# Performance work log

Hardware: AMD Instinct MI355X
Metric: run time of the kernel (lower is better)

Reference implementation:

```python
import math
import jax
import jax.numpy as jnp
import numpy as np
from jax import lax

D_MODEL = 256
N = 64
L = 2048
BATCH = 8
DT = 0.1


def setup_inputs() -> dict:
    key = jax.random.key(0)
    k1, k2, k3, k4 = jax.random.split(key, 4)
    n2 = N // 2
    # Faithful parameter init from _init_parameters
    A_real = jnp.log(jnp.ones((D_MODEL, n2), jnp.float32) * 0.5)
    A_imag = jnp.broadcast_to(jnp.arange(n2, dtype=jnp.float32) * math.pi, (D_MODEL, n2))
    C_real = jax.random.normal(k1, (D_MODEL, n2), jnp.float32)
    C_imag = jax.random.normal(k2, (D_MODEL, n2), jnp.float32)
    D = jnp.zeros((D_MODEL,), jnp.float32)
    u = jax.random.normal(k3, (BATCH, L, D_MODEL), jnp.float32)
    return {"u": u, "A_real": A_real, "A_imag": A_imag,
            "C_real": C_real, "C_imag": C_imag, "D": D}


def reference(u, A_real, A_imag, C_real, C_imag, D):
    batch, Lseq, d_model = u.shape
    # A = -exp(A_real) + i*A_imag ; discretize: A_disc = exp(A * dt)
    A = (-jnp.exp(A_real) + 1j * A_imag).astype(jnp.complex64)
    A_disc = jnp.exp(A * DT)  # (d, n/2) complex
    C = (C_real + 1j * C_imag).astype(jnp.complex64)  # (d, n/2)
    # torch.fft.rfftfreq(2L, 1/L) = arange(L+1) / 2
    freqs = jnp.arange(Lseq + 1, dtype=jnp.float32) * 0.5
    omega = jnp.exp((-2j * math.pi) * freqs.astype(jnp.complex64) / Lseq)  # (L+1,)
    # Cauchy-like sum over modes: (d, n/2, L+1) -> (d, L+1)
    k_f = (C[:, :, None] / (1.0 - omega[None, None, :] * A_disc[:, :, None])).sum(axis=1)
    # irfft to length 2L, keep first L taps -> depthwise conv kernel (d, L)
    k = jnp.fft.irfft(k_f, n=2 * Lseq, axis=-1)[:, :Lseq].astype(u.dtype)
    pad_left = (Lseq - 1) // 2
    pad_right =Seq = Lseq // 2
    uT = jnp.transpose(u, (0, 2, 1))  # (B, d, L)
    # torch conv1d == cross-correlation == lax conv (no kernel flip)
    y = lax.conv_general_dilated(
        uT, k[:, None, :],  # (d, 1, L) depthwise kernel
        window_strides=(1,), padding=[(pad_left, pad_right)],
        feature_group_count=d_model,
        dimension_numbers=("NCH", "OIH", "NCH"))
    y = y + D[None, :, None]
    return jnp.transpose(y, (0, 2, 1))  # (B, L, d)
```

## Files before the change

kernel.cpp:

```cpp
#include <hip/hip_runtime.h>
#include <hip/hip_bf16.h>
#include <math.h>

#define LSEQ   2048
#define DMODEL 256
#define NHALF  32
#define TMAX   1024
#define TM2    384
#define KPAD   16
#define KROWS  (LSEQ + 2*KPAD)
#define TT     16

typedef __attribute__((ext_vector_type(8))) short short8;
typedef __attribute__((ext_vector_type(4))) float f32x4;
typedef __attribute__((ext_vector_type(4))) unsigned int u32x4;

#define U3STR   2120
#define U3SH    (8*U3STR)
#define U3BYTES (U3SH*2)
#define KSLOT_STR 8848
#define OFF_K    U3BYTES
#define SMEM_F3  (OFF_K + 8*KSLOT_STR)
#define KBF_SH   4400
#define YTR_SMEM (64*260*4)
#define UIMG_SHORTS ((size_t)DMODEL*U3SH)
#define KBF_OFF_SH  UIMG_SHORTS
#define YT_OFF_B    ((UIMG_SHORTS + (size_t)DMODEL*KBF_SH)*2)
#define WS_NEED3    (YT_OFF_B + (size_t)8*LSEQ*DMODEL*4)

#define PB_CT0 0
#define PB_CT1 4928
#define PB_HRE 9856
#define PB_HIE 11392
#define PB_HIO 12160
#define PB_P   12928
#define PB_Q   17280
#define PB_C   23808
#define PB_BYTES 33792

__global__ __launch_bounds__(512, 2) void s4d_prep(
    const float* __restrict__ u,
    const float* __restrict__ A_real, const float* __restrict__ A_imag,
    const float* __restrict__ C_real, const float* __restrict__ C_imag,
    unsigned short* __restrict__ uimg, unsigned short* __restrict__ kbf)
{
    __shared__ __align__(16) unsigned char pbuf[PB_BYTES];
    const int tid = threadIdx.x;

    if (blockIdx.y < 8) {
        unsigned short (*tr)[66] = (unsigned short (*)[66])pbuf;
        const int m0 = blockIdx.x * 64;
        const int b  = blockIdx.y;

        const int mmBase = tid >> 6;
        const int d4     = (tid & 63) * 4;
        #pragma unroll
        for (int it = 0; it < 8; ++it) {
            int mm = it*8 + mmBase;
            const float* src = u + ((size_t)b*LSEQ + m0 + mm)*DMODEL + d4;
            f32x4 v = *(const f32x4*)src;
            #pragma unroll
            for (int j = 0; j < 4; ++j) {
                __hip_bfloat16 hb = __float2bfloat16(v[j]);
                tr[d4+j][mm] = *(unsigned short*)&hb;
            }
        }
        __syncthreads();
        #pragma unroll
        for (int P = 0; P < 4; ++P) {
            int d = P*64 + (tid >> 3);
            int c = tid & 7;
            const unsigned short* s = &tr[d][c*8];
            u32x4 w = { *(const unsigned*)(s),   *(const unsigned*)(s+2),
                        *(const unsigned*)(s+4), *(const unsigned*)(s+6) };
            *(u32x4*)(uimg + (size_t)d*U3SH + (size_t)b*U3STR + 32 + m0 + c*8) = w;
        }
        if (blockIdx.x == 0 && tid < 256) {
            int d = tid;
            #pragma unroll
            for (int c = 0; c < 4; ++c)
                *(u32x4*)(uimg + (size_t)d*U3SH + (size_t)b*U3STR + c*8) = (u32x4){0,0,0,0};
        } else if (blockIdx.x == 31 && tid < 256) {
            int d = tid;
            #pragma unroll
            for (int c = 0; c < 5; ++c)
                *(u32x4*)(uimg + (size_t)d*U3SH + (size_t)b*U3STR + 2080 + c*8) = (u32x4){0,0,0,0};
        }
    } else {
        const int d = (blockIdx.y - 8)*32 + blockIdx.x;
        float* ctL0 = (float*)(pbuf + PB_CT0);
        float* ctL1 = (float*)(pbuf + PB_CT1);
        float* hRe  = (float*)(pbuf + PB_HRE);
        float* hImE = (float*)(pbuf + PB_HIE);
        float* hImO = (float*)(pbuf + PB_HIO);
        float* Pp   = (float*)(pbuf + PB_P);
        float* Qp   = (float*)(pbuf + PB_Q);
        float* Cp   = (float*)(pbuf + PB_C);

        for (int i = tid; i < 1220; i += 512) {
            int x0 = (i - 196) & 2047;
            int x1 = (i - 195) & 2047;
            float a0 = (float)(M_PI/(2.0*(double)LSEQ)) * (float)(2*x0 + 1);
            float a1 = (float)(M_PI/(2.0*(double)LSEQ)) * (float)(2*x1 + 1);
            float s0, c0, s1, c1;
            sincosf(a0, &s0, &c0);
            sincosf(a1, &s1, &c1);
            ctL0[i] = c0 / s0;
            ctL1[i] = c1 / s1;
        }
        if (tid < 32) {
            const int n = tid;
            float ar = A_real[d*NHALF + n], ai = A_imag[d*NHALF + n];
            float cr = C_real[d*NHALF + n], ci = C_imag[d*NHALF + n];
            float amp = expf(-0.1f * expf(ar));
            float sn, cs; sincosf(0.1f * ai, &sn, &cs);
            float Adr = amp*cs, Adi = amp*sn;
            float pr = 1.f, pi = 0.f;
            Pp[n*2] = pr; Pp[n*2 + 1] = pi;
            #pragma unroll
            for (int i = 1; i < 16; ++i) {
                float nr = pr*Adr - pi*Adi;
                float ni = pr*Adi + pi*Adr;
                pr = nr; pi = ni;
                Pp[i*68 + n*2] = pr; Pp[i*68 + n*2 + 1] = pi;
            }
            float a16r = pr*Adr - pi*Adi;
            float a16i = pr*Adi + pi*Adr;
            float qr = 1.f, qi = 0.f;
            Qp[n*2] = qr; Qp[n*2 + 1] = qi;
            #pragma unroll
            for (int j = 1; j < 24; ++j) {
                float nr = qr*a16r - qi*a16i;
                float ni = qr*a16i + qi*a16r;
                qr = nr; qi = ni;
                Qp[j*68 + n*2] = qr; Qp[j*68 + n*2 + 1] = qi;
            }
            Cp[n*2] = cr; Cp[n*2 + 1] = ci;
        }
        __syncthreads();

        if (tid < TM2) {
            const int tau = tid, ii = tau & 15, jj = tau >> 4;
            const float* Pr = Pp + ii*68;
            const float* Qr = Qp + jj*68;
            float aR = 0.f, aI = 0.f;
            #pragma unroll 4
            for (int n = 0; n < 32; n += 2) {
                f32x4 p = *(const f32x4*)(Pr + 2*n);
                f32x4 q = *(const f32x4*)(Qr + 2*n);
                f32x4 c = *(const f32x4*)(Cp + 2*n);
                float w0r = p[0]*q[0] - p[1]*q[1];
                float w0i = p[0]*q[1] + p[1]*q[0];
                aR = fmaf(c[0], w0r, aR); aR = fmaf(-c[1], w0i, aR);
                aI = fmaf(c[0], w0i, aI); aI = fmaf( c[1], w0r, aI);
                float w1r = p[2]*q[2] - p[3]*q[3];
                float w1i = p[2]*q[3] + p[3]*q[2];
                aR = fmaf(c[2], w1r, aR); aR = fmaf(-c[3], w1i, aR);
                aI = fmaf(c[2], w1i, aI); aI = fmaf( c[3], w1r, aI);
            }
            hRe[tau] = aR;
            if (tau & 1) hImO[tau >> 1] = aI;
            else         hImE[tau >> 1] = aI;
        }
        __syncthreads();

        unsigned short* kd = kbf + (size_t)d*KBF_SH;
        {
            const int pt = tid & 1;
            const int g  = tid >> 1;
            const float* tb = pt ? ctL1 : ctL0;
            const float* hb = pt ? hImE : hImO;

            float acc0 = 0.f, acc1 = 0.f, acc2 = 0.f, acc3 = 0.f;
            int qb = 4*g + 192;
            f32x4 Wlo = *(const f32x4*)(tb + qb);
            f32x4 Whi = *(const f32x4*)(tb + qb + 4);

            #pragma unroll 4
            for (int R = 0; R < 48; ++R) {
                f32x4 hv = *(const f32x4*)(hb + 4*R);
                f32x4 Wn = *(const f32x4*)(tb + qb - 4);
                acc0 = fmaf(Wlo[3], hv[0], acc0); acc1 = fmaf(Whi[0], hv[0], acc1);
                acc2 = fmaf(Whi[1], hv[0], acc2); acc3 = fmaf(Whi[2], hv[0], acc3);
                acc0 = fmaf(Wlo[2], hv[1], acc0); acc1 = fmaf(Wlo[3], hv[1], acc1);
                acc2 = fmaf(Whi[0], hv[1], acc2); acc3 = fmaf(Whi[1], hv[1], acc3);
                acc0 = fmaf(Wlo[1], hv[2], acc0); acc1 = fmaf(Wlo[2], hv[2], acc1);
                acc2 = fmaf(Wlo[3], hv[2], acc2); acc3 = fmaf(Whi[0], hv[2], acc3);
                acc0 = fmaf(Wlo[0], hv[3], acc0); acc1 = fmaf(Wlo[1], hv[3], acc1);
                acc2 = fmaf(Wlo[2], hv[3], acc2); acc3 = fmaf(Wlo[3], hv[3], acc3);
                Whi = Wlo; Wlo = Wn; qb -= 4;
            }

            float accs[4] = {acc0, acc1, acc2, acc3};
            #pragma unroll
            for (int e = 0; e < 4; ++e) {
                int t = 8*g + 2*e + pt;
                float base = (t < TM2) ? hRe[t] : 0.f;
                float kv = base - accs[e] * (1.0f/(float)LSEQ);
                __hip_bfloat16 hbv = __float2bfloat16(kv);
                kd[1056 + t] = *(unsigned short*)&hbv;
            }
        }
        if (tid < 132) *(u32x4*)((unsigned char*)kd + tid*16) = (u32x4){0,0,0,0};
        if (tid < 162) *(u32x4*)((unsigned char*)kd + 6208 + tid*16) = (u32x4){0,0,0,0};
    }
}

#define MF(a, b, c) __builtin_amdgcn_mfma_f32_16x16x32_bf16((a), (b), (c), 0, 0, 0)

#define BODY(P) do {                                                        \
    const short8 bcur = Bb[(P) & 3];                                        \
    Bb[((P)+2) & 3] = *(const short8*)(sm + aBn);                           \
    acc[7] = MF(A[((P)+1) & 7], bcur, acc[7]);                              \
    A[((P)+1) & 7] = *(const short8*)(sm + aAn);                            \
    aAn += 64; aBn += 64;                                                   \
    acc[6] = MF(A[((P)+2) & 7], bcur, acc[6]);                              \
    acc[5] = MF(A[((P)+3) & 7], bcur, acc[5]);                              \
    acc[4] = MF(A[((P)+4) & 7], bcur, acc[4]);                              \
    acc[3] = MF(A[((P)+5) & 7], bcur, acc[3]);                              \
    acc[2] = MF(A[((P)+6) & 7], bcur, acc[2]);                              \
    acc[1] = MF(A[((P)+7) & 7], bcur, acc[1]);                              \
    acc[0] = MF(A[(P) & 7],     bcur, acc[0]);                              \
} while (0)

__global__ __launch_bounds__(512, 1) void s4d_mfma9(
    const unsigned short* __restrict__ uimg, const unsigned short* __restrict__ kbf,
    const float* __restrict__ Dvec, float* __restrict__ yT)
{
    extern __shared__ __align__(16) unsigned char sm[];
    const int tid = threadIdx.x;
    const int Bk  = blockIdx.x;
    const int d   = ((Bk & 7) << 5) | (Bk >> 3);

    const u32x4* gu = (const u32x4*)(uimg + (size_t)d*U3SH);
    const u32x4* gk = (const u32x4*)(kbf + (size_t)d*KBF_SH);
    u32x4 stg[5], kst[2];
    #pragma unroll
    for (int r = 0; r < 5; ++r) {
        int i = tid + 512*r;
        if (i < U3SH/8) stg[r] = gu[i];
    }
    #pragma unroll
    for (int r = 0; r < 2; ++r) {
        int i = tid + 512*r;
        if (i < KBF_SH/8) kst[r] = gk[i];
    }
    #pragma unroll
    for (int r = 0; r < 5; ++r) {
        int i = tid + 512*r;
        if (i < U3SH/8) *(u32x4*)(sm + i*16) = stg[r];
    }
    #pragma unroll
    for (int r = 0; r < 2; ++r) {
        int i = tid + 512*r;
        if (i < KBF_SH/8) *(u32x4*)(sm + OFF_K + i*16) = kst[r];
    }
    __syncthreads();

    {
        const unsigned short* s0p = (const unsigned short*)(sm + OFF_K);
        for (int i = tid; i < 548; i += 512) {
            int z0 = i*8;
            u32x4 va = *(const u32x4*)(s0p + z0);
            u32x4 vb = *(const u32x4*)(s0p + z0 + 8);
            unsigned src[8] = { va[0], va[1], va[2], va[3],
                                vb[0], vb[1], vb[2], vb[3] };
            #pragma unroll
            for (int c = 1; c < 8; ++c) {
                u32x4 w;
                if ((c & 1) == 0) {
                    int q = c >> 1;
                    w = (u32x4){ src[q], src[q+1], src[q+2], src[q+3] };
                } else {
                    int q = (c - 1) >> 1;
                    w = (u32x4){ (src[q]   >> 16) | (src[q+1] << 16),
                                 (src[q+1] >> 16) | (src[q+2] << 16),
                                 (src[q+2] >> 16) | (src[q+3] << 16),
                                 (src[q+3] >> 16) | (src[q+4] << 16) };
                }
                *(u32x4*)(sm + OFF_K + c*KSLOT_STR + z0*2) = w;
            }
        }
    }
    __syncthreads();

    const int lane = tid & 63, wv = tid >> 6;
    const int h    = lane >> 4;
    const int col  = lane & 15;
    const int t0w  = wv << 8;

    const int cA   = (7 - col) & 7;
    const int bA0  = OFF_K + cA*KSLOT_STR + 2*(2047 + 8*h - col - cA - t0w);
    const int laneB3 = (col & 7)*(U3STR*2) + 64 + 16*h + 32*(col >> 3);

    const float dv = Dvec[d];
    f32x4 acc[8];
    #pragma unroll
    for (int j = 0; j < 8; ++j) acc[j] = (f32x4){dv, dv, dv, dv};

    short8 A[8], Bb[4];
    #pragma unroll
    for (int w = 0; w < 8; ++w)
        A[w] = *(const short8*)(sm + bA0 - 64*((8 - w) & 7));
    Bb[0] = *(const short8*)(sm + laneB3 - 64);
    Bb[1] = *(const short8*)(sm + laneB3);

    int aAn = bA0 + 64;
    int aBn = laneB3 + 64;

    BODY(0);
    for (int o = 0; o < 8; ++o) {
        BODY(1); BODY(2); BODY(3); BODY(4);
        BODY(5); BODY(6); BODY(7); BODY(0);
    }

    {
        const int b    = col & 7;
        const int hi16 = (col >> 3) << 4;
        float* yb = yT + (size_t)d*(8*LSEQ) + (size_t)b*LSEQ;
        #pragma unroll
        for (int j = 0; j < 8; ++j) {
            int trow = t0w + 32*j + hi16 + 4*h;
            *(f32x4*)(yb + trow) = acc[j];
        }
    }
}

__global__ __launch_bounds__(256) void s4d_ytr(const float* __restrict__ yT,
                                               float* __restrict__ out)
{
    extern __shared__ float tr2[];
    const int tid = threadIdx.x;
    const int t0  = blockIdx.x * 64;
    const int b   = blockIdx.y;

    const int g = tid >> 4, i = tid & 15;
    #pragma unroll
    for (int dp = 0; dp < 16; ++dp) {
        int dd = dp*16 + g;
        f32x4 v = *(const f32x4*)(yT + (size_t)dd*(8*LSEQ) + (size_t)b*LSEQ + t0 + i*4);
        tr2[(i*4+0)*260 + dd] = v[0];
        tr2[(i*4+1)*260 + dd] = v[1];
        tr2[(i*4+2)*260 + dd] = v[2];
        tr2[(i*4+3)*260 + dd] = v[3];
    }
    __syncthreads();
    const int d4 = (tid & 63)*4, ttB = tid >> 6;
    #pragma unroll
    for (int s = 0; s < 16; ++s) {
        int tt = s*4 + ttB;
        f32x4 w = *(const f32x4*)(tr2 + tt*260 + d4);
        *(f32x4*)(out + ((size_t)b*LSEQ + t0 + tt)*DMODEL + d4) = w;
    }
}

__global__ __launch_bounds__(256) void s4d_build_k(
    const float* __restrict__ A_real, const float* __restrict__ A_imag,
    const float* __restrict__ C_real, const float* __restrict__ C_imag,
    float* __restrict__ kT)
{
    __shared__ float hRe[TMAX], hIm[TMAX], ct[LSEQ], prm[4][NHALF];
    const int tid = threadIdx.x;
    const int d   = blockIdx.x;
    if (tid < NHALF) {
        prm[0][tid] = A_real[d*NHALF + tid];
        prm[1][tid] = A_imag[d*NHALF + tid];
        prm[2][tid] = C_real[d*NHALF + tid];
        prm[3][tid] = C_imag[d*NHALF + tid];
    }
    #pragma unroll
    for (int r = 0; r < LSEQ/256; ++r) {
        int i = tid + 256*r;
        float ang = (float)(M_PI/(2.0*(double)LSEQ)) * (float)(2*i + 1);
        float sv, cv; sincosf(ang, &sv, &cv);
        ct[i] = cv / sv;
    }
    __syncthreads();
    for (int r = 0; r < TMAX/256; ++r) {
        int tau = tid + 256*r;
        float aR = 0.f, aI = 0.f;
        for (int n = 0; n < NHALF; ++n) {
            float lr  = -expf(prm[0][n]) * 0.1f;
            float amp = expf(lr * (float)tau);
            double ph = (double)prm[1][n] * 0.1 * (double)tau;
            ph -= floor(ph * (1.0/(2.0*M_PI))) * (2.0*M_PI);
            float sv, cv; sincosf((float)ph, &sv, &cv);
            float cr = prm[2][n], ci = prm[3][n];
            aR = fmaf(amp, cr*cv - ci*sv, aR);
            aI = fmaf(amp, cr*sv + ci*cv, aI);
        }
        hRe[tau] = aR; hIm[tau] = aI;
    }
    __syncthreads();
    float base[8], hsum[8];
    #pragma unroll
    for (int r = 0; r < 8; ++r) {
        base[r] = (r < 4) ? hRe[tid + 256*r] : 0.f;
        hsum[r] = 0.f;
    }
    const int tau0 = (tid & 1) ^ 1;
    for (int tau = tau0; tau < TMAX; tau += 2) {
        float him = hIm[tau];
        #pragma unroll
        for (int r = 0; r < 8; ++r) {
            int idx = ((tid + 256*r - tau) & (2*LSEQ - 1)) >> 1;
            hsum[r] = fmaf(ct[idx], him, hsum[r]);
        }
    }
    #pragma unroll
    for (int r = 0; r < 8; ++r) {
        int t = tid + 256*r;
        kT[(t + KPAD)*DMODEL + d] = base[r] - hsum[r] * (1.0f/(float)LSEQ);
    }
    if (tid < 2*KPAD) {
        int row = (tid < KPAD) ? tid : (LSEQ + KPAD + (tid - KPAD));
        kT[row*DMODEL + d] = 0.f;
    }
}

__global__ __launch_bounds__(256) void s4d_conv(
    const float* __restrict__ u, const float* __restrict__ Dvec,
    const float* __restrict__ kT, float* __restrict__ out)
{
    const int d  = threadIdx.x;
    const int t0 = blockIdx.x * TT;
    const int b  = blockIdx.y;
    float dvv = Dvec[d];
    float acc[TT];
    #pragma unroll
    for (int i = 0; i < TT; ++i) acc[i] = dvv;
    const float* ub   = u + (size_t)b * LSEQ * DMODEL + d;
    const float* kcol = kT + d;
    int mstart = t0 - 1024; if (mstart < 0) mstart = 0;
    int mend   = t0 + 1040; if (mend > LSEQ) mend = LSEQ;
    float kreg[31];
    {
        int jpb = mstart - t0 + 1024;
        #pragma unroll
        for (int r = 0; r < 31; ++r) kreg[r] = kcol[(jpb + r)*DMODEL];
    }
    for (int m0 = mstart; m0 < mend; m0 += TT) {
        float ureg[TT];
        #pragma unroll
        for (int mm = 0; mm < TT; ++mm) ureg[mm] = ub[(m0 + mm)*DMODEL];
        float knew[TT];
        if (m0 + TT < mend) {
            int jnb = m0 - t0 + 1024 + 31;
            #pragma unroll
            for (int r = 0; r < TT; ++r) knew[r] = kcol[(jnb + r)*DMODEL];
        } else {
            #pragma unroll
            for (int r = 0; r < TT; ++r) knew[r] = 0.f;
        }
        #pragma unroll
        for (int mm = 0; mm < TT; ++mm)
            #pragma unroll
            for (int tt = 0; tt < TT; ++tt)
                acc[tt] = fmaf(ureg[mm], kreg[mm - tt + 15], acc[tt]);
        #pragma unroll
        for (int r = 0; r < 15; ++r) kreg[r] = kreg[r + 16];
        #pragma unroll
        for (int r = 0; r < 16; ++r) kreg[15 + r] = knew[r];
    }
    float* ob = out + ((size_t)b * LSEQ + t0) * DMODEL + d;
    #pragma unroll
    for (int tt = 0; tt < TT; ++tt) ob[tt*DMODEL] = acc[tt];
}

extern "C" void kernel_launch(void* const* d_in, const int* in_sizes, int n_in,
                              void* d_out, int out_size, void* d_ws, size_t ws_size,
                              hipStream_t stream)
{
    const float* u  = (const float*)d_in[0];
    const float* Ar = (const float*)d_in[1];
    const float* Ai = (const float*)d_in[2];
    const float* Cr = (const float*)d_in[3];
    const float* Ci = (const float*)d_in[4];
    const float* Dv = (const float*)d_in[5];
    float* out = (float*)d_out;
    int B = in_sizes[0] / (LSEQ * DMODEL);

    if (B == 8 && ws_size >= WS_NEED3) {
        unsigned short* uimg = (unsigned short*)d_ws;
        unsigned short* kbf  = uimg + KBF_OFF_SH;
        float* yT = (float*)((unsigned char*)d_ws + YT_OFF_B);
        hipFuncSetAttribute((const void*)s4d_mfma9,
                            hipFuncAttributeMaxDynamicSharedMemorySize, SMEM_F3);
        hipFuncSetAttribute((const void*)s4d_ytr,
                            hipFuncAttributeMaxDynamicSharedMemorySize, YTR_SMEM);
        s4d_prep<<<dim3(32, 16), 512, 0, stream>>>(u, Ar, Ai, Cr, Ci, uimg, kbf);
        s4d_mfma9<<<DMODEL, 512, SMEM_F3, stream>>>(uimg, kbf, Dv, yT);
        s4d_ytr<<<dim3(LSEQ/64, 8), 256, YTR_SMEM, stream>>>(yT, out);
    } else {
        float* kT = (float*)d_ws;
        s4d_build_k<<<DMODEL, 256, 0, stream>>>(Ar, Ai, Cr, Ci, kT);
        s4d_conv<<<dim3(LSEQ/TT, B), 256, 0, stream>>>(u, Dv, kT, out);
    }
}
```

Baseline: 40.03 us.

## Stream B operand from global memory and split each channel across two blocks

The convolution MFMA kernel stops staging the bf16 u-image in shared memory and loads the B operand straight from global memory inside the inner loop. Each channel is now handled by two 256-thread blocks, each covering half of the output time range, which doubles the grid to 512 blocks. This removes the large u staging copy and cuts LDS use to the shifted-kernel slots only, so more blocks can be resident per CU. In exchange, the hot loop now waits on global/L2 latency for B, and every block rebuilds the shifted kernel copies, duplicating that setup work.

Measured after the change: 44.78 us. +11.9%, slower.

```diff
diff --git a/kernel.cpp b/kernel.cpp
--- a/kernel.cpp
+++ b/kernel.cpp
@@ -17,10 +17,8 @@
 
 #define U3STR   2120
 #define U3SH    (8*U3STR)
-#define U3BYTES (U3SH*2)
 #define KSLOT_STR 8848
-#define OFF_K    U3BYTES
-#define SMEM_F3  (OFF_K + 8*KSLOT_STR)
+#define SMEM_F4  (8*KSLOT_STR)
 #define KBF_SH   4400
 #define YTR_SMEM (64*260*4)
 #define UIMG_SHORTS ((size_t)DMODEL*U3SH)
@@ -210,10 +208,10 @@
 
 #define BODY(P) do {                                                        \
     const short8 bcur = Bb[(P) & 3];                                        \
-    Bb[((P)+2) & 3] = *(const short8*)(sm + aBn);                           \
+    Bb[((P)+2) & 3] = *(const short8*)(gBn);                                \
     acc[7] = MF(A[((P)+1) & 7], bcur, acc[7]);                              \
     A[((P)+1) & 7] = *(const short8*)(sm + aAn);                            \
-    aAn += 64; aBn += 64;                                                   \
+    aAn += 64; gBn += 32;                                                   \
     acc[6] = MF(A[((P)+2) & 7], bcur, acc[6]);                              \
     acc[5] = MF(A[((P)+3) & 7], bcur, acc[5]);                              \
     acc[4] = MF(A[((P)+4) & 7], bcur, acc[4]);                              \
@@ -223,43 +221,33 @@
     acc[0] = MF(A[(P) & 7],     bcur, acc[0]);                              \
 } while (0)
 
-__global__ __launch_bounds__(512, 1) void s4d_mfma9(
+__global__ __launch_bounds__(256, 2) void s4d_mfma10(
     const unsigned short* __restrict__ uimg, const unsigned short* __restrict__ kbf,
     const float* __restrict__ Dvec, float* __restrict__ yT)
 {
     extern __shared__ __align__(16) unsigned char sm[];
     const int tid = threadIdx.x;
-    const int Bk  = blockIdx.x;
-    const int d   = ((Bk & 7) << 5) | (Bk >> 3);
-
-    const u32x4* gu = (const u32x4*)(uimg + (size_t)d*U3SH);
+    const int v    = ((blockIdx.x & 7) << 6) | (blockIdx.x >> 3);
+    const int d    = v >> 1;
+    const int half = v & 1;
+
     const u32x4* gk = (const u32x4*)(kbf + (size_t)d*KBF_SH);
-    u32x4 stg[5], kst[2];
-    #pragma unroll
-    for (int r = 0; r < 5; ++r) {
-        int i = tid + 512*r;
-        if (i < U3SH/8) stg[r] = gu[i];
-    }
-    #pragma unroll
-    for (int r = 0; r < 2; ++r) {
-        int i = tid + 512*r;
+    u32x4 kst[3];
+    #pragma unroll
+    for (int r = 0; r < 3; ++r) {
+        int i = tid + 256*r;
         if (i < KBF_SH/8) kst[r] = gk[i];
     }
     #pragma unroll
-    for (int r = 0; r < 5; ++r) {
-        int i = tid + 512*r;
-        if (i < U3SH/8) *(u32x4*)(sm + i*16) = stg[r];
-    }
-    #pragma unroll
-    for (int r = 0; r < 2; ++r) {
-        int i = tid + 512*r;
-        if (i < KBF_SH/8) *(u32x4*)(sm + OFF_K + i*16) = kst[r];
+    for (int r = 0; r < 3; ++r) {
+        int i = tid + 256*r;
+        if (i < KBF_SH/8) *(u32x4*)(sm + i*16) = kst[r];
     }
     __syncthreads();
 
     {
-        const unsigned short* s0p = (const unsigned short*)(sm + OFF_K);
-        for (int i = tid; i < 548; i += 512) {
+        const unsigned short* s0p = (const unsigned short*)sm;
+        for (int i = tid; i < 548; i += 256) {
             int z0 = i*8;
             u32x4 va = *(const u32x4*)(s0p + z0);
             u32x4 vb = *(const u32x4*)(s0p + z0 + 8);
@@ -278,7 +266,7 @@
                                  (src[q+2] >> 16) | (src[q+3] << 16),
                                  (src[q+3] >> 16) | (src[q+4] << 16) };
                 }
-                *(u32x4*)(sm + OFF_K + c*KSLOT_STR + z0*2) = w;
+                *(u32x4*)(sm + c*KSLOT_STR + z0*2) = w;
             }
         }
     }
@@ -287,11 +275,12 @@
     const int lane = tid & 63, wv = tid >> 6;
     const int h    = lane >> 4;
     const int col  = lane & 15;
-    const int t0w  = wv << 8;
-
-    const int cA   = (7 - col) & 7;
-    const int bA0  = OFF_K + cA*KSLOT_STR + 2*(2047 + 8*h - col - cA - t0w);
-    const int laneB3 = (col & 7)*(U3STR*2) + 64 + 16*h + 32*(col >> 3);
+    const int t0w  = (half*4 + wv) << 8;
+
+    const int cA  = (7 - col) & 7;
+    const int bA0 = cA*KSLOT_STR + 2*(2047 + 8*h - col - cA - t0w);
+    const unsigned short* gB = uimg + (size_t)d*U3SH + (size_t)(col & 7)*U3STR
+                             + 8*h + 16*(col >> 3);
 
     const float dv = Dvec[d];
     f32x4 acc[8];
@@ -302,11 +291,11 @@
     #pragma unroll
     for (int w = 0; w < 8; ++w)
         A[w] = *(const short8*)(sm + bA0 - 64*((8 - w) & 7));
-    Bb[0] = *(const short8*)(sm + laneB3 - 64);
-    Bb[1] = *(const short8*)(sm + laneB3);
+    Bb[0] = *(const short8*)(gB);
+    Bb[1] = *(const short8*)(gB + 32);
 
     int aAn = bA0 + 64;
-    int aBn = laneB3 + 64;
+    const unsigned short* gBn = gB + 64;
 
     BODY(0);
     for (int o = 0; o < 8; ++o) {
@@ -484,12 +473,12 @@
         unsigned short* uimg = (unsigned short*)d_ws;
         unsigned short* kbf  = uimg + KBF_OFF_SH;
         float* yT = (float*)((unsigned char*)d_ws + YT_OFF_B);
-        hipFuncSetAttribute((const void*)s4d_mfma9,
-                            hipFuncAttributeMaxDynamicSharedMemorySize, SMEM_F3);
+        hipFuncSetAttribute((const void*)s4d_mfma10,
+                            hipFuncAttributeMaxDynamicSharedMemorySize, SMEM_F4);
         hipFuncSetAttribute((const void*)s4d_ytr,
                             hipFuncAttributeMaxDynamicSharedMemorySize, YTR_SMEM);
         s4d_prep<<<dim3(32, 16), 512, 0, stream>>>(u, Ar, Ai, Cr, Ci, uimg, kbf);
-        s4d_mfma9<<<DMODEL, 512, SMEM_F3, stream>>>(uimg, kbf, Dv, yT);
+        s4d_mfma10<<<512, 256, SMEM_F4, stream>>>(uimg, kbf, Dv, yT);
         s4d_ytr<<<dim3(LSEQ/64, 8), 256, YTR_SMEM, stream>>>(yT, out);
     } else {
         float* kT = (float*)d_ws;
```
